# Performance work log

Measured on AMD Instinct MI355X. Metric: run time of the kernel, lower is better.

## Reference

```python
import jax, jax.numpy as jnp
import numpy as np
from jax import lax

NUM_EXPERT = 2   # top-k experts kept per image
N_EXPERTS = 4    # total experts


def setup_inputs() -> dict:
    key = jax.random.key(0)
    ks = jax.random.split(key, 4)
    B, C, H, W = 16, 64, 128, 128
    inputs = jax.random.normal(ks[0], (B, C, H, W), dtype=jnp.float32)
    k = jax.random.uniform(ks[1], (B, C, 1, 1), dtype=jnp.float32)
    gate_w = jax.random.normal(ks[2], (N_EXPERTS, C), dtype=jnp.float32) * (1.0 / np.sqrt(C))
    gate_b = jnp.zeros((N_EXPERTS,), dtype=jnp.float32)
    conv_w = jax.random.normal(ks[3], (N_EXPERTS, C, C, 3, 3), dtype=jnp.float32) * (1.0 / np.sqrt(C * 9))
    conv_b = jnp.zeros((N_EXPERTS, C), dtype=jnp.float32)
    return {"inputs": inputs, "k": k, "gate_w": gate_w, "gate_b": gate_b,
            "conv_w": conv_w, "conv_b": conv_b}


def _expert(x, k, w, b):
    # expert_i(x, k) = ReLU(Conv3x3_i(x) + b_i) * k   (FiLM-style conditioning)
    y = lax.conv_general_dilated(x, w, window_strides=(1, 1), padding='SAME',
                                 dimension_numbers=('NCHW', 'OIHW', 'NCHW'))
    return jax.nn.relu(y + b[None, :, None, None]) * k


def reference(inputs, k, gate_w, gate_b, conv_w, conv_b):
    B = inputs.shape[0]
    # gate: global average pool over HW, then linear C -> E
    pooled = inputs.mean(axis=(2, 3))                       # [B, C]
    logits = pooled @ gate_w.T + gate_b                     # [B, E]
    # softmax in float32 (matches F.softmax(..., dtype=torch.float))
    weights = jax.nn.softmax(logits.astype(jnp.float32), axis=1).astype(inputs.dtype)
    topk_w, topk_idx = lax.top_k(weights, NUM_EXPERT)       # [B, num_expert]
    # scatter top-k weights into a dense [B, E] mask (zeros elsewhere)
    exp_weights = jnp.zeros_like(weights).at[jnp.arange(B)[:, None], topk_idx].set(topk_w)
    # dense loop over ALL experts, weighted sum with mostly-zero weights
    out = inputs
    for i in range(N_EXPERTS):
        out = out + _expert(inputs, k, conv_w[i], conv_b[i]) * exp_weights[:, i, None, None, None]
    return out
```

## Files before the change

kernel.cpp:

```cpp
#include <hip/hip_runtime.h>

typedef __attribute__((ext_vector_type(8))) short bfrag8;
typedef __attribute__((ext_vector_type(4))) short bfrag4;
typedef __attribute__((ext_vector_type(16))) float f32x16;

#define B_ 16
#define C_ 64
#define H_ 128
#define W_ 128
#define E_ 4
#define HW_ (H_ * W_)

#define PLANE 2080
#define ROWB  16640
#define RG 4

#define WT_ELEMS (4 * 9 * 2 * 4 * 64 * 8)
#define OFF_POOL (WT_ELEMS * 2)
#define OFF_EW   (OFF_POOL + 1024 * 4)
#define WS_NEEDED ((size_t)(OFF_EW + 64 * 4))

#define FB_WT_OFF 0
#define FB_POOLED_OFF 147456
#define FB_EW_OFF 148480

__device__ inline unsigned short f2bf(float f) {
    unsigned u = __builtin_bit_cast(unsigned, f);
    unsigned r = u + 0x7FFFu + ((u >> 16) & 1u);
    return (unsigned short)(r >> 16);
}
__device__ inline float bf2f(unsigned short s) {
    return __builtin_bit_cast(float, (unsigned)s << 16);
}

__global__ __launch_bounds__(256) void pool_wcvt(const float* __restrict__ in,
                                                 const float* __restrict__ cw,
                                                 float* __restrict__ pooled,
                                                 unsigned short* __restrict__ wT2) {
    if (blockIdx.x < 576) {
        const int idx = blockIdx.x * 256 + threadIdx.x;
        const int j = idx & 7;
        const int l = (idx >> 3) & 63;
        const int f = idx >> 9;
        const int kb = f & 3;
        const int chh = (f >> 2) & 1;
        const int et = f >> 3;
        const int tap = et % 9;
        const int e = et / 9;
        const int co = chh * 32 + (l & 31);
        const int ci = kb * 16 + (l >> 5) * 8 + j;
        wT2[idx] = f2bf(cw[(((e * C_ + co) * C_ + ci) * 9) + tap]);
    }
    const int bc = blockIdx.x;
    const float* p = in + (size_t)bc * HW_;
    float s = 0.f;
    for (int i = threadIdx.x; i < HW_ / 4; i += 256) {
        float4 v = ((const float4*)p)[i];
        s += v.x + v.y + v.z + v.w;
    }
    for (int off = 32; off; off >>= 1) s += __shfl_down(s, off);
    __shared__ float red[4];
    const int lane = threadIdx.x & 63, wv = threadIdx.x >> 6;
    if (lane == 0) red[wv] = s;
    __syncthreads();
    if (threadIdx.x == 0)
        pooled[bc] = (red[0] + red[1] + red[2] + red[3]) * (1.0f / (float)HW_);
}

__global__ void gate_kernel(const float* __restrict__ pooled,
                            const float* __restrict__ gate_w,
                            const float* __restrict__ gate_b,
                            float* __restrict__ ew) {
    const int b = threadIdx.x;
    if (b >= B_) return;
    float lg[E_];
    for (int e = 0; e < E_; e++) {
        float s = gate_b[e];
        for (int c = 0; c < C_; c++) s += pooled[b * C_ + c] * gate_w[e * C_ + c];
        lg[e] = s;
    }
    float m = fmaxf(fmaxf(lg[0], lg[1]), fmaxf(lg[2], lg[3]));
    float ex[E_], sum = 0.f;
    for (int e = 0; e < E_; e++) { ex[e] = expf(lg[e] - m); sum += ex[e]; }
    for (int e = 0; e < E_; e++) ex[e] /= sum;
    int i1 = 0;
    for (int e = 1; e < E_; e++) if (ex[e] > ex[i1]) i1 = e;
    int i2 = -1;
    for (int e = 0; e < E_; e++) {
        if (e == i1) continue;
        if (i2 < 0 || ex[e] > ex[i2]) i2 = e;
    }
    for (int e = 0; e < E_; e++)
        ew[b * E_ + e] = (e == i1 || e == i2) ? ex[e] : 0.f;
}

__global__ __launch_bounds__(512, 2) void conv_x2(const float* __restrict__ in,
                                                  const float* __restrict__ kk,
                                                  const float* __restrict__ cb,
                                                  const float* __restrict__ ew,
                                                  const unsigned short* __restrict__ wT2,
                                                  float* __restrict__ out) {
    const int raw = blockIdx.x;
    const int swz = (raw & 7) * 64 + (raw >> 3);
    const int b = swz >> 5;
    const int h0 = (swz & 31) * RG;
    const int tid = threadIdx.x;
    const int lane = tid & 63;
    const int wv = tid >> 6;
    const int ln = lane & 31;
    const int lh = lane >> 5;
    const int ch = wv & 1;
    const int co0 = ch * 32;
    const int x0 = (wv >> 1) * 32;

    const int px = tid & 127;
    const int cg = tid >> 7;

    __shared__ __align__(16) char ring[3 * ROWB];

    int e0 = 0, e1 = 0; float w0 = 0.f, w1 = 0.f;
    {
        int found = 0;
        for (int e = 0; e < E_; e++) {
            float we = ew[b * E_ + e];
            if (we != 0.f) {
                if (!found) { e0 = e; w0 = we; found = 1; }
                else        { e1 = e; w1 = we; }
            }
        }
        if (w1 == 0.f) e1 = e0;
    }

    float pv[16];

    auto STAGE = [&](int r) {
        if ((unsigned)r < (unsigned)H_) {
            const float* src = in + ((size_t)(b * C_ + cg * 16) * H_ + r) * W_ + px;
#pragma unroll
            for (int i = 0; i < 16; ++i) pv[i] = src[(size_t)i * HW_];
        } else {
#pragma unroll
            for (int i = 0; i < 16; ++i) pv[i] = 0.f;
        }
    };
    auto COMMIT = [&](int rs) {
        char* bp = ring + rs * ROWB + (px + 1) * 16;
        bfrag8 f0, f1;
#pragma unroll
        for (int j = 0; j < 8; ++j) {
            f0[j] = (short)f2bf(pv[j]);
            f1[j] = (short)f2bf(pv[8 + j]);
        }
        *(bfrag8*)(bp + (2 * cg) * PLANE) = f0;
        *(bfrag8*)(bp + (2 * cg + 1) * PLANE) = f1;
    };

    if (tid < 48) {
        const int r = tid >> 4;
        const int c = tid & 15;
        const int chh = c >> 1;
        const int sl = (c & 1) ? 129 : 0;
        const bfrag8 z = {0, 0, 0, 0, 0, 0, 0, 0};
        *(bfrag8*)(ring + r * ROWB + chh * PLANE + sl * 16) = z;
    }

    STAGE(h0 - 1); COMMIT(0);
    STAGE(h0);     COMMIT(1);
    STAGE(h0 + 1); COMMIT(2);
    __syncthreads();

    const char* wbase0 = (const char*)wT2 + (size_t)e0 * 9 * 8192 + ch * 4096 + lane * 16;
    const char* wbase1 = (const char*)wT2 + (size_t)e1 * 9 * 8192 + ch * 4096 + lane * 16;

    int m0 = 0, m1 = 1, m2 = 2;
    for (int s = 0; s < RG; ++s) {
        if (s + 1 < RG) STAGE(h0 + s + 2);

        f32x16 A0, A1;
#pragma unroll
        for (int i = 0; i < 16; ++i) { A0[i] = 0.f; A1[i] = 0.f; }

#pragma unroll 1
        for (int ky = 0; ky < 3; ++ky) {
            const char* rb = ring + (ky == 0 ? m0 : (ky == 1 ? m1 : m2)) * ROWB + (x0 + ln) * 16;
            const char* wk0 = wbase0 + ky * 24576;
            const char* wk1 = wbase1 + ky * 24576;
#pragma unroll 1
            for (int kx = 0; kx < 3; ++kx) {
#pragma unroll
                for (int kb = 0; kb < 4; ++kb) {
                    bfrag8 a0 = *(const bfrag8*)(wk0 + kx * 8192 + kb * 1024);
                    bfrag8 a1 = *(const bfrag8*)(wk1 + kx * 8192 + kb * 1024);
                    bfrag8 bb = *(const bfrag8*)(rb + (2 * kb + lh) * PLANE + kx * 16);
                    A0 = __builtin_amdgcn_mfma_f32_32x32x16_bf16(a0, bb, A0, 0, 0, 0);
                    A1 = __builtin_amdgcn_mfma_f32_32x32x16_bf16(a1, bb, A1, 0, 0, 0);
                }
            }
        }

        __syncthreads();
        if (s + 1 < RG) COMMIT(m0);

        const int row = h0 + s;
        const char* rm1 = ring + m1 * ROWB + (x0 + ln + 1) * 16 + lh * 8;
        bfrag4 ra[4];
#pragma unroll
        for (int c = 0; c < 4; ++c)
            ra[c] = *(const bfrag4*)(rm1 + (co0 / 8 + c) * PLANE);
#pragma unroll
        for (int rg = 0; rg < 16; ++rg) {
            const int r = rg & 3, c = rg >> 2;
            const int co = co0 + r + 8 * c + 4 * lh;
            const float kv = kk[b * C_ + co];
            const float bb0 = cb[e0 * C_ + co], bb1 = cb[e1 * C_ + co];
            const size_t base = ((size_t)(b * C_ + co) * H_ + row) * W_ + x0 + ln;
            out[base] = bf2f((unsigned short)ra[c][r])
                        + fmaxf(A0[rg] + bb0, 0.f) * (kv * w0)
                        + fmaxf(A1[rg] + bb1, 0.f) * (kv * w1);
        }

        __syncthreads();
        const int t = m0; m0 = m1; m1 = m2; m2 = t;
    }
}

#define CHUNK 32

__global__ __launch_bounds__(256) void pool_kernel(const float* __restrict__ in,
                                                   float* __restrict__ pooled) {
    const int bc = blockIdx.x;
    const float* p = in + (size_t)bc * HW_;
    float s = 0.f;
    for (int i = threadIdx.x; i < HW_ / 4; i += 256) {
        float4 v = ((const float4*)p)[i];
        s += v.x + v.y + v.z + v.w;
    }
    for (int off = 32; off; off >>= 1) s += __shfl_down(s, off);
    __shared__ float red[4];
    const int lane = threadIdx.x & 63, wv = threadIdx.x >> 6;
    if (lane == 0) red[wv] = s;
    __syncthreads();
    if (threadIdx.x == 0)
        pooled[bc] = (red[0] + red[1] + red[2] + red[3]) * (1.0f / (float)HW_);
}

__global__ __launch_bounds__(256) void wtr_kernel(const float* __restrict__ cw,
                                                  float* __restrict__ wT) {
    const int idx = blockIdx.x * 256 + threadIdx.x;
    if (idx >= E_ * C_ * 9 * C_) return;
    const int co = idx & 63;
    const int t2 = idx >> 6;
    const int tap = t2 % 9;
    const int t3 = t2 / 9;
    const int ci = t3 & 63;
    const int e = t3 >> 6;
    wT[idx] = cw[(((e * C_ + co) * C_ + ci) * 9) + tap];
}

__global__ __launch_bounds__(512) void conv_fallback(const float* __restrict__ in,
                                                     const float* __restrict__ kk,
                                                     const float* __restrict__ wT,
                                                     const float* __restrict__ cb,
                                                     const float* __restrict__ ew,
                                                     float* __restrict__ out) {
    const int bid = blockIdx.x;
    const int b = bid / H_;
    const int h = bid % H_;
    const int tid = threadIdx.x;
    const int lane = tid & 63;
    const int wv = tid >> 6;
    const int x0 = wv * 16;

    __shared__ float sIn[CHUNK * 3 * W_];

    float w0 = 0.f, w1 = 0.f;
    int e0 = 0, e1 = 0;
    {
        float we[E_];
#pragma unroll
        for (int e = 0; e < E_; e++) we[e] = ew[b * E_ + e];
        int found = 0;
        for (int e = 0; e < E_; e++) {
            if (we[e] != 0.f) {
                if (!found) { e0 = e; w0 = we[e]; found = 1; }
                else        { e1 = e; w1 = we[e]; }
            }
        }
        if (w1 == 0.f) e1 = e0;
    }

    float acc0[16], acc1[16];
#pragma unroll
    for (int i = 0; i < 16; i++) { acc0[i] = 0.f; acc1[i] = 0.f; }

    for (int cblk = 0; cblk < C_ / CHUNK; cblk++) {
        const int cbase = cblk * CHUNK;
        __syncthreads();
        for (int f = tid; f < CHUNK * 3 * W_ / 4; f += 512) {
            const int fi = f * 4;
            const int ci = fi / (3 * W_);
            const int rem = fi - ci * 3 * W_;
            const int kyy = rem / W_;
            const int x = rem - kyy * W_;
            const int hh = h + kyy - 1;
            float4 v = make_float4(0.f, 0.f, 0.f, 0.f);
            if (hh >= 0 && hh < H_)
                v = *(const float4*)(in + ((size_t)(b * C_ + cbase + ci) * H_ + hh) * W_ + x);
            *(float4*)(sIn + fi) = v;
        }
        __syncthreads();

        const float* wp0 = wT + (size_t)((e0 * C_ + cbase) * 9) * C_ + lane;
        const float* wp1 = wT + (size_t)((e1 * C_ + cbase) * 9) * C_ + lane;
        for (int ci = 0; ci < CHUNK; ci++) {
            float wa[9], wb[9];
#pragma unroll
            for (int t = 0; t < 9; t++) {
                wa[t] = wp0[(ci * 9 + t) * C_];
                wb[t] = wp1[(ci * 9 + t) * C_];
            }
            const float* rowp = sIn + ci * 3 * W_;
#pragma unroll
            for (int kyy = 0; kyy < 3; kyy++) {
                float xin[18];
                const float* rp = rowp + kyy * W_ + x0;
                xin[0] = (x0 == 0) ? 0.f : rp[-1];
#pragma unroll
                for (int j = 0; j < 16; j += 4) {
                    float4 v = *(const float4*)(rp + j);
                    xin[1 + j] = v.x; xin[2 + j] = v.y; xin[3 + j] = v.z; xin[4 + j] = v.w;
                }
                xin[17] = (x0 + 16 >= W_) ? 0.f : rp[16];
                const int t0 = kyy * 3;
#pragma unroll
                for (int x = 0; x < 16; x++) {
                    acc0[x] += xin[x] * wa[t0] + xin[x + 1] * wa[t0 + 1] + xin[x + 2] * wa[t0 + 2];
                    acc1[x] += xin[x] * wb[t0] + xin[x + 1] * wb[t0 + 1] + xin[x + 2] * wb[t0 + 2];
                }
            }
        }
    }

    const float kv = kk[b * C_ + lane];
    const float b0v = cb[e0 * C_ + lane];
    const float b1v = cb[e1 * C_ + lane];
    const float kw0 = kv * w0, kw1 = kv * w1;
    const size_t obase = ((size_t)(b * C_ + lane) * H_ + h) * W_ + x0;
#pragma unroll
    for (int x = 0; x < 16; x += 4) {
        float4 iv = *(const float4*)(in + obase + x);
        float4 ov;
        ov.x = iv.x + fmaxf(acc0[x + 0] + b0v, 0.f) * kw0 + fmaxf(acc1[x + 0] + b1v, 0.f) * kw1;
        ov.y = iv.y + fmaxf(acc0[x + 1] + b0v, 0.f) * kw0 + fmaxf(acc1[x + 1] + b1v, 0.f) * kw1;
        ov.z = iv.z + fmaxf(acc0[x + 2] + b0v, 0.f) * kw0 + fmaxf(acc1[x + 2] + b1v, 0.f) * kw1;
        ov.w = iv.w + fmaxf(acc0[x + 3] + b0v, 0.f) * kw0 + fmaxf(acc1[x + 3] + b1v, 0.f) * kw1;
        *(float4*)(out + obase + x) = ov;
    }
}

extern "C" void kernel_launch(void* const* d_in, const int* in_sizes, int n_in,
                              void* d_out, int out_size, void* d_ws, size_t ws_size,
                              hipStream_t stream) {
    const float* inputs = (const float*)d_in[0];
    const float* k      = (const float*)d_in[1];
    const float* gate_w = (const float*)d_in[2];
    const float* gate_b = (const float*)d_in[3];
    const float* conv_w = (const float*)d_in[4];
    const float* conv_b = (const float*)d_in[5];
    float* out = (float*)d_out;
    char* wsb = (char*)d_ws;

    if (ws_size >= WS_NEEDED) {
        unsigned short* wT2 = (unsigned short*)wsb;
        float* pooled = (float*)(wsb + OFF_POOL);
        float* ewbuf  = (float*)(wsb + OFF_EW);

        pool_wcvt<<<B_ * C_, 256, 0, stream>>>(inputs, conv_w, pooled, wT2);
        gate_kernel<<<1, 64, 0, stream>>>(pooled, gate_w, gate_b, ewbuf);
        conv_x2<<<512, 512, 0, stream>>>(inputs, k, conv_b, ewbuf, wT2, out);
    } else {
        float* ws = (float*)d_ws;
        float* wTf    = ws + FB_WT_OFF;
        float* pooled = ws + FB_POOLED_OFF;
        float* ewbuf  = ws + FB_EW_OFF;

        pool_kernel<<<B_ * C_, 256, 0, stream>>>(inputs, pooled);
        gate_kernel<<<1, 64, 0, stream>>>(pooled, gate_w, gate_b, ewbuf);
        wtr_kernel<<<(E_ * C_ * 9 * C_ + 255) / 256, 256, 0, stream>>>(conv_w, wTf);
        conv_fallback<<<B_ * H_, 512, 0, stream>>>(inputs, k, wTf, conv_b, ewbuf, out);
    }
}
```

Baseline: 87.74 us.

## Keep conv weights in registers and split K across waves in conv kernel

The conv kernel is restructured so each wave holds its slice of both selected experts' weights in registers for the whole block, instead of reloading weight fragments from global memory on every tap. The input-channel reduction is split across two wave groups; one group writes bf16-packed partial sums into the output buffer and the other reads them back and finishes the epilogue. Tiles become 64 pixels wide by 16 rows, with halo columns staged explicitly, and the grid halves to 256 blocks at one block per CU. The cost is high register pressure, an extra global round-trip with bf16 rounding of partial sums, and lower occupancy.

```diff
diff --git a/kernel.cpp b/kernel.cpp
--- a/kernel.cpp
+++ b/kernel.cpp
@@ -11,9 +11,10 @@
 #define E_ 4
 #define HW_ (H_ * W_)
 
-#define PLANE 2080
-#define ROWB  16640
-#define RG 4
+#define NSL 66
+#define PLANE2 (NSL * 16)
+#define ROWB2  (8 * PLANE2)
+#define RGK 16
 
 #define WT_ELEMS (4 * 9 * 2 * 4 * 64 * 8)
 #define OFF_POOL (WT_ELEMS * 2)
@@ -94,29 +95,34 @@
         ew[b * E_ + e] = (e == i1 || e == i2) ? ex[e] : 0.f;
 }
 
-__global__ __launch_bounds__(512, 2) void conv_x2(const float* __restrict__ in,
-                                                  const float* __restrict__ kk,
-                                                  const float* __restrict__ cb,
-                                                  const float* __restrict__ ew,
-                                                  const unsigned short* __restrict__ wT2,
-                                                  float* __restrict__ out) {
+__global__ __launch_bounds__(512, 1) void conv_kreg(const float* __restrict__ in,
+                                                    const float* __restrict__ kk,
+                                                    const float* __restrict__ cb,
+                                                    const float* __restrict__ ew,
+                                                    const unsigned short* __restrict__ wT2,
+                                                    float* __restrict__ out) {
     const int raw = blockIdx.x;
-    const int swz = (raw & 7) * 64 + (raw >> 3);
-    const int b = swz >> 5;
-    const int h0 = (swz & 31) * RG;
+    const int swz = (raw & 7) * 32 + (raw >> 3);
+    const int b   = swz >> 4;
+    const int pxh = (swz >> 3) & 1;
+    const int rgp = swz & 7;
+    const int h0  = rgp * RGK;
+    const int x0g = pxh * 64;
+
     const int tid = threadIdx.x;
     const int lane = tid & 63;
     const int wv = tid >> 6;
     const int ln = lane & 31;
     const int lh = lane >> 5;
-    const int ch = wv & 1;
+    const int ksl = wv >> 2;
+    const int ch  = (wv >> 1) & 1;
+    const int pq  = wv & 1;
     const int co0 = ch * 32;
-    const int x0 = (wv >> 1) * 32;
-
-    const int px = tid & 127;
-    const int cg = tid >> 7;
-
-    __shared__ __align__(16) char ring[3 * ROWB];
+
+    const int spx = tid & 63;
+    const int scg = tid >> 6;
+
+    __shared__ __align__(16) char ring[3 * ROWB2];
 
     int e0 = 0, e1 = 0; float w0 = 0.f, w1 = 0.f;
     {
@@ -131,50 +137,63 @@
         if (w1 == 0.f) e1 = e0;
     }
 
-    float pv[16];
-
+    bfrag8 wr[2][9][2];
+    {
+        const char* wtb = (const char*)wT2 + ch * 4096 + (ksl * 2) * 1024 + lane * 16;
+#pragma unroll
+        for (int ei = 0; ei < 2; ++ei) {
+            const int es = ei ? e1 : e0;
+            const char* base = wtb + (size_t)es * 73728;
+#pragma unroll
+            for (int tap = 0; tap < 9; ++tap)
+#pragma unroll
+                for (int kw = 0; kw < 2; ++kw)
+                    wr[ei][tap][kw] = *(const bfrag8*)(base + tap * 8192 + kw * 1024);
+        }
+    }
+
+    float pv[8], ph[8];
     auto STAGE = [&](int r) {
         if ((unsigned)r < (unsigned)H_) {
-            const float* src = in + ((size_t)(b * C_ + cg * 16) * H_ + r) * W_ + px;
-#pragma unroll
-            for (int i = 0; i < 16; ++i) pv[i] = src[(size_t)i * HW_];
+            const float* src = in + ((size_t)(b * C_ + scg * 8) * H_ + r) * W_ + x0g + spx;
+#pragma unroll
+            for (int i = 0; i < 8; ++i) pv[i] = src[(size_t)i * HW_];
         } else {
 #pragma unroll
-            for (int i = 0; i < 16; ++i) pv[i] = 0.f;
+            for (int i = 0; i < 8; ++i) pv[i] = 0.f;
+        }
+        if (tid < 16) {
+            const int hp = tid & 1;
+            const int cgh = tid >> 1;
+            const int pg = hp ? (x0g + 64) : (x0g - 1);
+            const bool ok = ((unsigned)r < (unsigned)H_) && ((unsigned)pg < (unsigned)W_);
+            const float* src = in + ((size_t)(b * C_ + cgh * 8) * H_ + (((unsigned)r < (unsigned)H_) ? r : 0)) * W_ + (ok ? pg : 0);
+#pragma unroll
+            for (int i = 0; i < 8; ++i) ph[i] = ok ? src[(size_t)i * HW_] : 0.f;
         }
     };
     auto COMMIT = [&](int rs) {
-        char* bp = ring + rs * ROWB + (px + 1) * 16;
-        bfrag8 f0, f1;
-#pragma unroll
-        for (int j = 0; j < 8; ++j) {
-            f0[j] = (short)f2bf(pv[j]);
-            f1[j] = (short)f2bf(pv[8 + j]);
-        }
-        *(bfrag8*)(bp + (2 * cg) * PLANE) = f0;
-        *(bfrag8*)(bp + (2 * cg + 1) * PLANE) = f1;
+        bfrag8 f;
+#pragma unroll
+        for (int i = 0; i < 8; ++i) f[i] = (short)f2bf(pv[i]);
+        *(bfrag8*)(ring + rs * ROWB2 + scg * PLANE2 + (spx + 1) * 16) = f;
+        if (tid < 16) {
+            const int hp = tid & 1, cgh = tid >> 1;
+            bfrag8 g;
+#pragma unroll
+            for (int i = 0; i < 8; ++i) g[i] = (short)f2bf(ph[i]);
+            *(bfrag8*)(ring + rs * ROWB2 + cgh * PLANE2 + (hp ? 65 : 0) * 16) = g;
+        }
     };
-
-    if (tid < 48) {
-        const int r = tid >> 4;
-        const int c = tid & 15;
-        const int chh = c >> 1;
-        const int sl = (c & 1) ? 129 : 0;
-        const bfrag8 z = {0, 0, 0, 0, 0, 0, 0, 0};
-        *(bfrag8*)(ring + r * ROWB + chh * PLANE + sl * 16) = z;
-    }
 
     STAGE(h0 - 1); COMMIT(0);
     STAGE(h0);     COMMIT(1);
     STAGE(h0 + 1); COMMIT(2);
     __syncthreads();
 
-    const char* wbase0 = (const char*)wT2 + (size_t)e0 * 9 * 8192 + ch * 4096 + lane * 16;
-    const char* wbase1 = (const char*)wT2 + (size_t)e1 * 9 * 8192 + ch * 4096 + lane * 16;
-
     int m0 = 0, m1 = 1, m2 = 2;
-    for (int s = 0; s < RG; ++s) {
-        if (s + 1 < RG) STAGE(h0 + s + 2);
+    for (int s = 0; s < RGK; ++s) {
+        if (s + 1 < RGK) STAGE(h0 + s + 2);
 
         f32x16 A0, A1;
 #pragma unroll
@@ -182,44 +201,53 @@
 
 #pragma unroll 1
         for (int ky = 0; ky < 3; ++ky) {
-            const char* rb = ring + (ky == 0 ? m0 : (ky == 1 ? m1 : m2)) * ROWB + (x0 + ln) * 16;
-            const char* wk0 = wbase0 + ky * 24576;
-            const char* wk1 = wbase1 + ky * 24576;
-#pragma unroll 1
+            const char* rb = ring + (ky == 0 ? m0 : (ky == 1 ? m1 : m2)) * ROWB2;
+#pragma unroll
             for (int kx = 0; kx < 3; ++kx) {
 #pragma unroll
-                for (int kb = 0; kb < 4; ++kb) {
-                    bfrag8 a0 = *(const bfrag8*)(wk0 + kx * 8192 + kb * 1024);
-                    bfrag8 a1 = *(const bfrag8*)(wk1 + kx * 8192 + kb * 1024);
-                    bfrag8 bb = *(const bfrag8*)(rb + (2 * kb + lh) * PLANE + kx * 16);
-                    A0 = __builtin_amdgcn_mfma_f32_32x32x16_bf16(a0, bb, A0, 0, 0, 0);
-                    A1 = __builtin_amdgcn_mfma_f32_32x32x16_bf16(a1, bb, A1, 0, 0, 0);
+                for (int kw = 0; kw < 2; ++kw) {
+                    bfrag8 bb = *(const bfrag8*)(rb + (ksl * 4 + kw * 2 + lh) * PLANE2
+                                                 + (pq * 32 + ln + kx) * 16);
+                    A0 = __builtin_amdgcn_mfma_f32_32x32x16_bf16(wr[0][ky * 3 + kx][kw], bb, A0, 0, 0, 0);
+                    A1 = __builtin_amdgcn_mfma_f32_32x32x16_bf16(wr[1][ky * 3 + kx][kw], bb, A1, 0, 0, 0);
                 }
             }
         }
 
         __syncthreads();
-        if (s + 1 < RG) COMMIT(m0);
+        if (s + 1 < RGK) COMMIT(m0);
 
         const int row = h0 + s;
-        const char* rm1 = ring + m1 * ROWB + (x0 + ln + 1) * 16 + lh * 8;
-        bfrag4 ra[4];
-#pragma unroll
-        for (int c = 0; c < 4; ++c)
-            ra[c] = *(const bfrag4*)(rm1 + (co0 / 8 + c) * PLANE);
-#pragma unroll
-        for (int rg = 0; rg < 16; ++rg) {
-            const int r = rg & 3, c = rg >> 2;
-            const int co = co0 + r + 8 * c + 4 * lh;
-            const float kv = kk[b * C_ + co];
-            const float bb0 = cb[e0 * C_ + co], bb1 = cb[e1 * C_ + co];
-            const size_t base = ((size_t)(b * C_ + co) * H_ + row) * W_ + x0 + ln;
-            out[base] = bf2f((unsigned short)ra[c][r])
-                        + fmaxf(A0[rg] + bb0, 0.f) * (kv * w0)
-                        + fmaxf(A1[rg] + bb1, 0.f) * (kv * w1);
-        }
-
+        const int pxg = x0g + pq * 32 + ln;
+        if (ksl == 1) {
+#pragma unroll
+            for (int g = 0; g < 16; ++g) {
+                const int co = co0 + (g & 3) + 8 * (g >> 2) + 4 * lh;
+                const unsigned pk = (unsigned)f2bf(A0[g]) | ((unsigned)f2bf(A1[g]) << 16);
+                ((unsigned*)out)[((size_t)(b * C_ + co) * H_ + row) * W_ + pxg] = pk;
+            }
+        }
         __syncthreads();
+        if (ksl == 0) {
+            const char* rm1 = ring + m1 * ROWB2 + (pq * 32 + ln + 1) * 16 + lh * 8;
+            bfrag4 ra[4];
+#pragma unroll
+            for (int c = 0; c < 4; ++c)
+                ra[c] = *(const bfrag4*)(rm1 + (ch * 4 + c) * PLANE2);
+#pragma unroll
+            for (int g = 0; g < 16; ++g) {
+                const int r_ = g & 3, c_ = g >> 2;
+                const int co = co0 + r_ + 8 * c_ + 4 * lh;
+                const size_t oi = ((size_t)(b * C_ + co) * H_ + row) * W_ + pxg;
+                const unsigned pk = ((const unsigned*)out)[oi];
+                const float t0 = A0[g] + bf2f((unsigned short)(pk & 0xFFFFu));
+                const float t1 = A1[g] + bf2f((unsigned short)(pk >> 16));
+                const float kv = kk[b * C_ + co];
+                out[oi] = bf2f((unsigned short)ra[c_][r_])
+                          + fmaxf(t0 + cb[e0 * C_ + co], 0.f) * (kv * w0)
+                          + fmaxf(t1 + cb[e1 * C_ + co], 0.f) * (kv * w1);
+            }
+        }
         const int t = m0; m0 = m1; m1 = m2; m2 = t;
     }
 }
@@ -377,7 +405,7 @@
 
         pool_wcvt<<<B_ * C_, 256, 0, stream>>>(inputs, conv_w, pooled, wT2);
         gate_kernel<<<1, 64, 0, stream>>>(pooled, gate_w, gate_b, ewbuf);
-        conv_x2<<<512, 512, 0, stream>>>(inputs, k, conv_b, ewbuf, wT2, out);
+        conv_kreg<<<256, 512, 0, stream>>>(inputs, k, conv_b, ewbuf, wT2, out);
     } else {
         float* ws = (float*)d_ws;
         float* wTf    = ws + FB_WT_OFF;
```

Result: slower. 272.0 us (+210.0%).
